# Performance work log

Measured on AMD Instinct MI355X. Metric: run time of the kernel, lower is better.

## Reference

```python
import jax, jax.numpy as jnp
import numpy as np

BN_EPS = 1e-5


def binarize(x):
    # sign binarization with straight-through estimator (identity grad)
    return x + jax.lax.stop_gradient(jnp.sign(x) - x)


def conv2d(x, w, stride):
    # x: [N,C,H,W], w: [O,I,kh,kw], VALID padding (PyTorch default padding=0)
    return jax.lax.conv_general_dilated(
        x, w, window_strides=(stride, stride), padding='VALID',
        dimension_numbers=('NCHW', 'OIHW', 'NCHW'))


def batchnorm(x, gamma, beta, mean, var):
    inv = gamma / jnp.sqrt(var + BN_EPS)          # [C]
    return x * inv[None, :, None, None] + (beta - mean * inv)[None, :, None, None]


def setup_inputs() -> dict:
    key = jax.random.key(0)
    ks = jax.random.split(key, 20)
    B = 8192
    f32 = jnp.float32
    d = {
        'x': jax.random.normal(ks[0], (B, 1, 24, 54), f32),
        'conv1_w': jax.random.normal(ks[1], (32, 1, 3, 3), f32) * 0.3,
        'conv1_b': jax.random.normal(ks[2], (32,), f32) * 0.1,
        'bn1_gamma': 1.0 + 0.1 * jax.random.normal(ks[3], (32,), f32),
        'bn1_beta': 0.1 * jax.random.normal(ks[4], (32,), f32),
        'bn1_mean': 0.1 * jax.random.normal(ks[5], (32,), f32),
        'bn1_var': jax.random.uniform(ks[6], (32,), f32, 0.5, 1.5),
        'conv2_w': jax.random.normal(ks[7], (64, 32, 3, 3), f32) * 0.1,
        'conv2_b': jax.random.normal(ks[8], (64,), f32) * 0.1,
        'bn2_gamma': 1.0 + 0.1 * jax.random.normal(ks[9], (64,), f32),
        'bn2_beta': 0.1 * jax.random.normal(ks[10], (64,), f32),
        'bn2_mean': 0.1 * jax.random.normal(ks[11], (64,), f32),
        'bn2_var': jax.random.uniform(ks[12], (64,), f32, 0.5, 1.5),
        'lin_w': jax.random.normal(ks[13], (500, 3840), f32) * 0.02,
        'lin_b': jax.random.normal(ks[14], (500,), f32) * 0.1,
        'out_w': jax.random.normal(ks[15], (10, 500), f32) * 0.05,
        'out_b': jax.random.normal(ks[16], (10,), f32) * 0.1,
    }
    return d


def reference(x, conv1_w, conv1_b, bn1_gamma, bn1_beta, bn1_mean, bn1_var,
              conv2_w, conv2_b, bn2_gamma, bn2_beta, bn2_mean, bn2_var,
              lin_w, lin_b, out_w, out_b):
    # conv1: input channels (1) != 3 -> input binarized; weight binarized; float bias
    h = conv2d(binarize(x), binarize(conv1_w), 2) + conv1_b[None, :, None, None]
    h = jax.nn.relu(batchnorm(h, bn1_gamma, bn1_beta, bn1_mean, bn1_var))  # [B,32,11,26]
    # conv2: input channels (32) != 3 -> input binarized (values in {0,1} post-ReLU)
    h = conv2d(binarize(h), binarize(conv2_w), 2) + conv2_b[None, :, None, None]
    h = jax.nn.relu(batchnorm(h, bn2_gamma, bn2_beta, bn2_mean, bn2_var))  # [B,64,5,12]
    h = h.reshape(-1, 3840)
    # BinarizeLinear: in_features (3840, 500) != 784 -> input binarized
    h = jax.nn.relu(binarize(h) @ binarize(lin_w).T + lin_b[None, :])      # [B,500]
    y = binarize(h) @ binarize(out_w).T + out_b[None, :]                   # [B,10]
    return y
```

## Files before the change

kernel.cpp:

```cpp
#include <hip/hip_runtime.h>
#include <cstdint>

#define BN_EPS 1e-5f

static constexpr int NB = 8192;
static constexpr int JLIN = 500;

typedef int v4i  __attribute__((ext_vector_type(4)));
typedef int v16i __attribute__((ext_vector_type(16)));


__global__ __launch_bounds__(256) void pack_kernel(
    const float* __restrict__ conv1_w, const float* __restrict__ conv1_b,
    const float* __restrict__ conv2_w, const float* __restrict__ conv2_b,
    const float* __restrict__ lin_w, const float* __restrict__ lin_b,
    const float* __restrict__ out_w,
    const float* __restrict__ bn1_g, const float* __restrict__ bn1_b,
    const float* __restrict__ bn1_m, const float* __restrict__ bn1_v,
    const float* __restrict__ bn2_g, const float* __restrict__ bn2_b,
    const float* __restrict__ bn2_m, const float* __restrict__ bn2_v,
    uint4* __restrict__ wbfrag, uint32_t* __restrict__ cdat,
    uint32_t* __restrict__ lut, uint32_t* __restrict__ wout,
    int* __restrict__ Tlin)
{
    __shared__ float    s_c1w[288];
    __shared__ uint32_t s_wp[32];
    __shared__ float    s_inv1[32], s_sh1[32], s_b1[32];

    int tid = threadIdx.x;
    int b   = blockIdx.x;

    if (b < 512) {
        int e  = b * 256 + tid;
        int L  = e & 63;
        int kq = (e >> 6) & 127;
        int jt = e >> 13;
        int j  = jt * 32 + (L & 31);
        int h  = L >> 5;
        uint32_t dd[4] = {0u, 0u, 0u, 0u};
        if (j < JLIN) {
            int c  = kq >> 1, hi = kq & 1;
            int nb = (hi ? 28 : 32) - 16 * h;
            const float* src = lin_w + (size_t)j * 3840 + c * 60 + hi * 32 + 16 * h;
            #pragma unroll
            for (int i = 0; i < 16; ++i) {
                uint32_t byte = 0;
                if (i < nb) byte = (src[i] > 0.0f) ? 0x01u : 0xFFu;
                dd[i >> 2] |= byte << (8 * (i & 3));
            }
        }
        wbfrag[e] = make_uint4(dd[0], dd[1], dd[2], dd[3]);
        return;
    }

    int mb = b - 512;
    if (mb < 2) {
        for (int i = tid; i < 288; i += 256) s_c1w[i] = conv1_w[i];
        __syncthreads();
        if (tid < 32) {
            uint32_t wp = 0;
            for (int t = 0; t < 9; ++t)
                wp |= (s_c1w[tid * 9 + t] < 0.0f ? 1u : 0u) << t;
            s_wp[tid] = wp;
            float inv = bn1_g[tid] / sqrtf(bn1_v[tid] + BN_EPS);
            s_inv1[tid] = inv;
            s_sh1[tid]  = bn1_b[tid] - bn1_m[tid] * inv;
            s_b1[tid]   = conv1_b[tid];
        }
        __syncthreads();
        uint32_t px = (uint32_t)(mb * 256 + tid);
        uint32_t word = 0;
        for (int c = 0; c < 32; ++c) {
            int d = 9 - 2 * __popc(px ^ s_wp[c]);
            float z = __fadd_rn((float)d, s_b1[c]);
            z = __fadd_rn(__fmul_rn(z, s_inv1[c]), s_sh1[c]);
            word |= (z > 0.0f ? 1u : 0u) << c;
        }
        lut[px] = word;
        return;
    }

    int idx = (mb - 2) * 256 + tid;
    if (idx < 576) {
        int c = idx / 9, tap = idx % 9;
        uint32_t w = 0;
        for (int ic = 0; ic < 32; ++ic)
            w |= (conv2_w[c * 288 + ic * 9 + tap] > 0.0f ? 1u : 0u) << ic;
        float inv = bn2_g[c] / sqrtf(bn2_v[c] + BN_EPS);
        if (inv < 0.0f) w = ~w;
        cdat[tap * 64 + c] = w;
    } else if (idx < 576 + 64) {
        int c = idx - 576;
        float inv = bn2_g[c] / sqrtf(bn2_v[c] + BN_EPS);
        float sh  = bn2_b[c] - bn2_m[c] * inv;
        float b2  = conv2_b[c];
        int T = 10000;
        for (int u = -300; u <= 300; ++u) {
            float v = (inv < 0.0f) ? (float)(-u) : (float)u;
            float z = __fadd_rn(__fmul_rn(__fadd_rn(v, b2), inv), sh);
            if (z > 0.0f) { T = u; break; }
        }
        cdat[576 + c] = (uint32_t)T;
    } else if (idx < 576 + 64 + 512) {
        int j = idx - (576 + 64);
        int T = 10000;
        if (j < JLIN) {
            float lb = lin_b[j];
            int base = (int)floorf(-lb) - 2;
            for (int u = base; u <= base + 5; ++u)
                if (__fadd_rn((float)u, lb) > 0.0f) { T = u; break; }
        }
        Tlin[j] = T;
    } else if (idx < 576 + 64 + 512 + 160) {
        int t = idx - (576 + 64 + 512);
        int j = t >> 4, k = t & 15;
        uint32_t w = 0;
        for (int bb = 0; bb < 32; ++bb) {
            int jj = k * 32 + bb;
            if (jj < JLIN) w |= (out_w[j * 500 + jj] > 0.0f ? 1u : 0u) << bb;
        }
        wout[t] = w;
    }
}

__global__ __launch_bounds__(256) void conv_kernel(
    const float* __restrict__ x,
    const uint32_t* __restrict__ cdat,
    const uint32_t* __restrict__ lut,
    uint32_t* __restrict__ h2b, int* __restrict__ Bs)
{
    __shared__ __align__(8) uint32_t s_flat[4][44];
    __shared__ uint32_t s_lut[512];
    __shared__ __align__(8) uint32_t s_in[4][288];
    __shared__ uint32_t s_base[4][64];

    int tid  = threadIdx.x;
    int lane = tid & 63;
    int wv   = tid >> 6;
    int s    = blockIdx.x * 4 + wv;

    s_lut[tid]       = lut[tid];
    s_lut[tid + 256] = lut[tid + 256];

    const float* xs = x + (size_t)s * 1296;
    #pragma unroll
    for (int it = 0; it < 21; ++it) {
        int f = it * 64 + lane;
        float v = (f < 1296) ? xs[f] : 1.0f;
        uint64_t mk = __ballot(v < 0.0f);
        if (lane == 0) *((uint64_t*)&s_flat[wv][2 * it]) = mk;
    }
    __syncthreads();

    for (int i = tid; i < 4 * 286; i += 256) {
        int sl = i / 286, p = i - sl * 286;
        int oy = p / 26, ox = p - oy * 26;
        uint32_t pxb = 0;
        #pragma unroll
        for (int ky = 0; ky < 3; ++ky) {
            int bitpos = 54 * (2 * oy + ky) + 2 * ox;
            int d  = bitpos >> 5;
            int sh = bitpos & 31;
            uint64_t wp = (uint64_t)s_flat[sl][d] | ((uint64_t)s_flat[sl][d + 1] << 32);
            pxb |= (((uint32_t)(wp >> sh)) & 7u) << (3 * ky);
        }
        s_in[sl][p] = s_lut[pxb];
    }
    __syncthreads();

    for (int i = tid; i < 4 * 60; i += 256) {
        int sl = i / 60, p = i - sl * 60;
        int oy = p / 12, ox = p - 12 * oy;
        uint32_t sum = 0;
        #pragma unroll
        for (int ky = 0; ky < 3; ++ky) {
            const uint32_t* rp = &s_in[sl][(2 * oy + ky) * 26 + 2 * ox];
            sum += __popc(rp[0]) + __popc(rp[1]) + __popc(rp[2]);
        }
        s_base[sl][p] = sum;
    }
    __syncthreads();

    int c = lane;
    uint32_t m[9];
    #pragma unroll
    for (int q = 0; q < 9; ++q) m[q] = cdat[q * 64 + c];
    int T = (int)cdat[576 + c];

    uint64_t acc = 0;
    for (int oy = 0; oy < 5; ++oy) {
        int P[12];
        #pragma unroll
        for (int ox = 0; ox < 12; ++ox) P[ox] = 0;
        #pragma unroll
        for (int ky = 0; ky < 3; ++ky) {
            const uint32_t* rp = &s_in[wv][(2 * oy + ky) * 26];
            uint32_t r[25];
            #pragma unroll
            for (int d = 0; d < 12; ++d)
                *(uint64_t*)&r[2 * d] = *(const uint64_t*)&rp[2 * d];
            r[24] = rp[24];
            uint32_t m0 = m[ky * 3 + 0], m1 = m[ky * 3 + 1], m2 = m[ky * 3 + 2];
            #pragma unroll
            for (int ox = 0; ox < 12; ++ox) {
                P[ox] += __popc(r[2 * ox]     & m0);
                P[ox] += __popc(r[2 * ox + 1] & m1);
                P[ox] += __popc(r[2 * ox + 2] & m2);
            }
        }
        const uint32_t* bp = &s_base[wv][oy * 12];
        uint32_t bits = 0;
        #pragma unroll
        for (int ox = 0; ox < 12; ++ox) {
            int v = 2 * P[ox] - (int)bp[ox];
            bits |= (v >= T ? 1u : 0u) << ox;
        }
        acc |= (uint64_t)bits << (12 * oy);
    }
    uint32_t w0 = (uint32_t)acc;
    uint32_t w1 = (uint32_t)(acc >> 32) & 0x0FFFFFFFu;

    int bsum = __popc(w0) + __popc(w1);
    #pragma unroll
    for (int off = 32; off > 0; off >>= 1) bsum += __shfl_xor(bsum, off, 64);
    if (lane == 0) Bs[s] = bsum;

    *(uint2*)(h2b + (size_t)s * 128 + 2 * c) = make_uint2(w0, w1);
}

__global__ __launch_bounds__(256) void lin2_kernel(
    const uint32_t* __restrict__ h2b,
    const uint4* __restrict__ wbfrag,
    const int* __restrict__ Tlin,
    uint32_t* __restrict__ h3w)
{
    __shared__ uint8_t As[64 * 520];

    int tid  = threadIdx.x;
    int lane = tid & 63;
    int wv   = __builtin_amdgcn_readfirstlane((int)(tid >> 6));
    int sblk = blockIdx.x >> 2;
    int jgrp = blockIdx.x & 3;
    int jt   = jgrp * 4 + wv;
    int s0   = sblk * 64;

    int T = Tlin[jt * 32 + (lane & 31)];
    int row  = lane & 31;
    int half = lane >> 5;

    v16i acc0 = {};
    v16i acc1 = {};

    for (int chunk = 0; chunk < 8; ++chunk) {
        for (int e = tid; e < 1024; e += 256) {
            int sm = e >> 4, wl = e & 15;
            uint32_t w = h2b[(size_t)(s0 + sm) * 128 + chunk * 16 + wl];
            uint32_t dw[8];
            #pragma unroll
            for (int q = 0; q < 8; ++q)
                dw[q] = (((w >> (4 * q)) & 0xFu) * 0x204081u) & 0x01010101u;
            uint64_t* dst = (uint64_t*)(As + sm * 520 + wl * 32);
            dst[0] = (uint64_t)dw[0] | ((uint64_t)dw[1] << 32);
            dst[1] = (uint64_t)dw[2] | ((uint64_t)dw[3] << 32);
            dst[2] = (uint64_t)dw[4] | ((uint64_t)dw[5] << 32);
            dst[3] = (uint64_t)dw[6] | ((uint64_t)dw[7] << 32);
        }
        __syncthreads();

        const uint4* bsrc = wbfrag + ((size_t)jt * 128 + chunk * 16) * 64 + lane;
        #pragma unroll 4
        for (int kq = 0; kq < 16; ++kq) {
            uint4 bw = bsrc[kq * 64];
            v4i bf = {(int)bw.x, (int)bw.y, (int)bw.z, (int)bw.w};
            const uint8_t* ap = As + row * 520 + kq * 32 + half * 16;
            uint64_t lo0 = *(const uint64_t*)ap;
            uint64_t hi0 = *(const uint64_t*)(ap + 8);
            const uint8_t* aq = ap + 32 * 520;
            uint64_t lo1 = *(const uint64_t*)aq;
            uint64_t hi1 = *(const uint64_t*)(aq + 8);
            v4i a0 = {(int)(uint32_t)lo0, (int)(lo0 >> 32),
                      (int)(uint32_t)hi0, (int)(hi0 >> 32)};
            v4i a1 = {(int)(uint32_t)lo1, (int)(lo1 >> 32),
                      (int)(uint32_t)hi1, (int)(hi1 >> 32)};
            acc0 = __builtin_amdgcn_mfma_i32_32x32x32_i8(a0, bf, acc0, 0, 0, 0);
            acc1 = __builtin_amdgcn_mfma_i32_32x32x32_i8(a1, bf, acc1, 0, 0, 0);
        }
        __syncthreads();
    }

    #pragma unroll
    for (int r = 0; r < 16; ++r) {
        int row0 = (r & 3) + 8 * (r >> 2);
        uint64_t mk0 = __ballot(acc0[r] >= T);
        uint64_t mk1 = __ballot(acc1[r] >= T);
        if (lane == 0) {
            h3w[(size_t)(s0 + row0) * 16 + jt]          = (uint32_t)mk0;
            h3w[(size_t)(s0 + row0 + 4) * 16 + jt]      = (uint32_t)(mk0 >> 32);
            h3w[(size_t)(s0 + 32 + row0) * 16 + jt]     = (uint32_t)mk1;
            h3w[(size_t)(s0 + 32 + row0 + 4) * 16 + jt] = (uint32_t)(mk1 >> 32);
        }
    }
}

__global__ __launch_bounds__(256) void out_kernel(
    const uint32_t* __restrict__ h3w,
    const uint32_t* __restrict__ wout,
    const float* __restrict__ out_b,
    float* __restrict__ out)
{
    int s = blockIdx.x * 256 + threadIdx.x;
    const uint4* hp = (const uint4*)(h3w + (size_t)s * 16);
    uint4 q0 = hp[0], q1 = hp[1], q2 = hp[2], q3 = hp[3];
    uint32_t w[16] = {q0.x, q0.y, q0.z, q0.w, q1.x, q1.y, q1.z, q1.w,
                      q2.x, q2.y, q2.z, q2.w, q3.x, q3.y, q3.z, q3.w};
    int B = 0;
    #pragma unroll
    for (int k = 0; k < 16; ++k) B += __popc(w[k]);
    #pragma unroll
    for (int o = 0; o < 10; ++o) {
        int P = 0;
        #pragma unroll
        for (int k = 0; k < 16; ++k) P += __popc(w[k] & wout[o * 16 + k]);
        out[(size_t)s * 10 + o] = __fadd_rn((float)(2 * P - B), out_b[o]);
    }
}

extern "C" void kernel_launch(void* const* d_in, const int* in_sizes, int n_in,
                              void* d_out, int out_size, void* d_ws, size_t ws_size,
                              hipStream_t stream)
{
    const float* x       = (const float*)d_in[0];
    const float* conv1_w = (const float*)d_in[1];
    const float* conv1_b = (const float*)d_in[2];
    const float* bn1_g   = (const float*)d_in[3];
    const float* bn1_b   = (const float*)d_in[4];
    const float* bn1_m   = (const float*)d_in[5];
    const float* bn1_v   = (const float*)d_in[6];
    const float* conv2_w = (const float*)d_in[7];
    const float* conv2_b = (const float*)d_in[8];
    const float* bn2_g   = (const float*)d_in[9];
    const float* bn2_b   = (const float*)d_in[10];
    const float* bn2_m   = (const float*)d_in[11];
    const float* bn2_v   = (const float*)d_in[12];
    const float* lin_w   = (const float*)d_in[13];
    const float* lin_b   = (const float*)d_in[14];
    const float* out_w   = (const float*)d_in[15];
    const float* out_b   = (const float*)d_in[16];

    char* ws = (char*)d_ws;
    uint32_t* h2b    = (uint32_t*)(ws + 0);
    uint4*    wbfrag = (uint4*)   (ws + 4194304);
    uint32_t* h3w    = (uint32_t*)(ws + 6291456);
    uint32_t* cdat   = (uint32_t*)(ws + 6815744);
    uint32_t* lut    = (uint32_t*)(ws + 6818304);
    uint32_t* wout   = (uint32_t*)(ws + 6820352);
    int*      Tlin   = (int*)     (ws + 6820992);
    int*      Bs     = (int*)     (ws + 6823040);

    pack_kernel<<<520, 256, 0, stream>>>(conv1_w, conv1_b, conv2_w, conv2_b,
                                         lin_w, lin_b, out_w,
                                         bn1_g, bn1_b, bn1_m, bn1_v,
                                         bn2_g, bn2_b, bn2_m, bn2_v,
                                         wbfrag, cdat, lut, wout, Tlin);
    conv_kernel<<<NB / 4, 256, 0, stream>>>(x, cdat, lut, h2b, Bs);
    lin2_kernel<<<512, 256, 0, stream>>>(h2b, wbfrag, Tlin, h3w);
    out_kernel<<<32, 256, 0, stream>>>(h3w, wout, out_b, (float*)d_out);
}
```

Measured before the change: 194.8 us.

## Move binary conv2 onto int8 MFMA with prepacked ±1 weight fragments

```diff
diff --git a/kernel.cpp b/kernel.cpp
--- a/kernel.cpp
+++ b/kernel.cpp
@@ -21,7 +21,7 @@
     const float* __restrict__ bn2_m, const float* __restrict__ bn2_v,
     uint4* __restrict__ wbfrag, uint32_t* __restrict__ cdat,
     uint32_t* __restrict__ lut, uint32_t* __restrict__ wout,
-    int* __restrict__ Tlin)
+    int* __restrict__ Tlin, uint4* __restrict__ wcfrag)
 {
     __shared__ float    s_c1w[288];
     __shared__ uint32_t s_wp[32];
@@ -50,6 +50,28 @@
             }
         }
         wbfrag[e] = make_uint4(dd[0], dd[1], dd[2], dd[3]);
+        return;
+    }
+
+    if (b >= 520) {
+        int e = (b - 520) * 256 + tid;
+        if (e < 1152) {
+            int t = e >> 7;
+            int n = (e >> 6) & 1;
+            int L = e & 63;
+            int c = n * 32 + (L & 31);
+            int hb = L >> 5;
+            bool flip = (bn2_g[c] < 0.0f);
+            uint32_t dd[4] = {0u, 0u, 0u, 0u};
+            #pragma unroll
+            for (int i = 0; i < 16; ++i) {
+                int ic = 16 * hb + i;
+                float w = conv2_w[c * 288 + ic * 9 + t];
+                uint32_t byte = ((w > 0.0f) == flip) ? 0xFFu : 0x01u;
+                dd[i >> 2] |= byte << (8 * (i & 3));
+            }
+            wcfrag[e] = make_uint4(dd[0], dd[1], dd[2], dd[3]);
+        }
         return;
     }
 
@@ -127,34 +149,38 @@
     const float* __restrict__ x,
     const uint32_t* __restrict__ cdat,
     const uint32_t* __restrict__ lut,
-    uint32_t* __restrict__ h2b, int* __restrict__ Bs)
-{
-    __shared__ __align__(8) uint32_t s_flat[4][44];
+    const uint4* __restrict__ wcfrag,
+    uint32_t* __restrict__ h2b)
+{
+    __shared__ __align__(16) uint8_t s_bytes[2 * 286 * 32];
     __shared__ uint32_t s_lut[512];
-    __shared__ __align__(8) uint32_t s_in[4][288];
-    __shared__ uint32_t s_base[4][64];
+    __shared__ __align__(8) uint32_t s_flat[2][44];
+    __shared__ uint64_t s_bal[2][2][2][16];
 
     int tid  = threadIdx.x;
     int lane = tid & 63;
     int wv   = tid >> 6;
-    int s    = blockIdx.x * 4 + wv;
+    int s0   = blockIdx.x * 2;
 
     s_lut[tid]       = lut[tid];
     s_lut[tid + 256] = lut[tid + 256];
 
-    const float* xs = x + (size_t)s * 1296;
-    #pragma unroll
-    for (int it = 0; it < 21; ++it) {
-        int f = it * 64 + lane;
-        float v = (f < 1296) ? xs[f] : 1.0f;
-        uint64_t mk = __ballot(v < 0.0f);
-        if (lane == 0) *((uint64_t*)&s_flat[wv][2 * it]) = mk;
+    {
+        int psl = wv >> 1, ph = wv & 1;
+        const float* xs = x + (size_t)(s0 + psl) * 1296;
+        int it0 = ph * 11, it1 = ph ? 21 : 11;
+        for (int it = it0; it < it1; ++it) {
+            int f = it * 64 + lane;
+            float v = (f < 1296) ? xs[f] : 1.0f;
+            uint64_t mk = __ballot(v < 0.0f);
+            if (lane == 0) *((uint64_t*)&s_flat[psl][2 * it]) = mk;
+        }
     }
     __syncthreads();
 
-    for (int i = tid; i < 4 * 286; i += 256) {
-        int sl = i / 286, p = i - sl * 286;
-        int oy = p / 26, ox = p - oy * 26;
+    for (int i = tid; i < 2 * 286; i += 256) {
+        int sl = i / 286, wnd = i - sl * 286;
+        int oy = wnd / 26, ox = wnd - oy * 26;
         uint32_t pxb = 0;
         #pragma unroll
         for (int ky = 0; ky < 3; ++ky) {
@@ -164,68 +190,69 @@
             uint64_t wp = (uint64_t)s_flat[sl][d] | ((uint64_t)s_flat[sl][d + 1] << 32);
             pxb |= (((uint32_t)(wp >> sh)) & 7u) << (3 * ky);
         }
-        s_in[sl][p] = s_lut[pxb];
+        uint32_t w = s_lut[pxb];
+        uint32_t dw[8];
+        #pragma unroll
+        for (int q = 0; q < 8; ++q)
+            dw[q] = (((w >> (4 * q)) & 0xFu) * 0x204081u) & 0x01010101u;
+        uint4* dst = (uint4*)(s_bytes + ((size_t)sl * 286 + wnd) * 32);
+        dst[0] = make_uint4(dw[0], dw[1], dw[2], dw[3]);
+        dst[1] = make_uint4(dw[4], dw[5], dw[6], dw[7]);
     }
     __syncthreads();
 
-    for (int i = tid; i < 4 * 60; i += 256) {
-        int sl = i / 60, p = i - sl * 60;
+    {
+        int sl = wv >> 1, rt = wv & 1;
+        int p = rt * 32 + (lane & 31);
+        if (p > 59) p = 59;
         int oy = p / 12, ox = p - 12 * oy;
-        uint32_t sum = 0;
-        #pragma unroll
-        for (int ky = 0; ky < 3; ++ky) {
-            const uint32_t* rp = &s_in[sl][(2 * oy + ky) * 26 + 2 * ox];
-            sum += __popc(rp[0]) + __popc(rp[1]) + __popc(rp[2]);
-        }
-        s_base[sl][p] = sum;
+        int hb = lane >> 5;
+        const uint8_t* abase = s_bytes + ((size_t)sl * 286 + 52 * oy + 2 * ox) * 32 + 16 * hb;
+        const uint4* bbase = wcfrag + lane;
+
+        v16i acc0 = {};
+        v16i acc1 = {};
+        #pragma unroll
+        for (int t = 0; t < 9; ++t) {
+            const int koff = (t / 3) * 26 + (t % 3);
+            uint4 av = *(const uint4*)(abase + koff * 32);
+            v4i af = {(int)av.x, (int)av.y, (int)av.z, (int)av.w};
+            uint4 b0 = bbase[t * 128];
+            uint4 b1 = bbase[t * 128 + 64];
+            v4i bf0 = {(int)b0.x, (int)b0.y, (int)b0.z, (int)b0.w};
+            v4i bf1 = {(int)b1.x, (int)b1.y, (int)b1.z, (int)b1.w};
+            acc0 = __builtin_amdgcn_mfma_i32_32x32x32_i8(af, bf0, acc0, 0, 0, 0);
+            acc1 = __builtin_amdgcn_mfma_i32_32x32x32_i8(af, bf1, acc1, 0, 0, 0);
+        }
+
+        int T0 = (int)cdat[576 + (lane & 31)];
+        int T1 = (int)cdat[576 + 32 + (lane & 31)];
+        #pragma unroll
+        for (int r = 0; r < 16; ++r) {
+            uint64_t m0 = __ballot(acc0[r] >= T0);
+            uint64_t m1 = __ballot(acc1[r] >= T1);
+            if (lane == 0) {
+                s_bal[sl][rt][0][r] = m0;
+                s_bal[sl][rt][1][r] = m1;
+            }
+        }
     }
     __syncthreads();
 
-    int c = lane;
-    uint32_t m[9];
-    #pragma unroll
-    for (int q = 0; q < 9; ++q) m[q] = cdat[q * 64 + c];
-    int T = (int)cdat[576 + c];
-
-    uint64_t acc = 0;
-    for (int oy = 0; oy < 5; ++oy) {
-        int P[12];
-        #pragma unroll
-        for (int ox = 0; ox < 12; ++ox) P[ox] = 0;
-        #pragma unroll
-        for (int ky = 0; ky < 3; ++ky) {
-            const uint32_t* rp = &s_in[wv][(2 * oy + ky) * 26];
-            uint32_t r[25];
-            #pragma unroll
-            for (int d = 0; d < 12; ++d)
-                *(uint64_t*)&r[2 * d] = *(const uint64_t*)&rp[2 * d];
-            r[24] = rp[24];
-            uint32_t m0 = m[ky * 3 + 0], m1 = m[ky * 3 + 1], m2 = m[ky * 3 + 2];
-            #pragma unroll
-            for (int ox = 0; ox < 12; ++ox) {
-                P[ox] += __popc(r[2 * ox]     & m0);
-                P[ox] += __popc(r[2 * ox + 1] & m1);
-                P[ox] += __popc(r[2 * ox + 2] & m2);
-            }
-        }
-        const uint32_t* bp = &s_base[wv][oy * 12];
-        uint32_t bits = 0;
-        #pragma unroll
-        for (int ox = 0; ox < 12; ++ox) {
-            int v = 2 * P[ox] - (int)bp[ox];
-            bits |= (v >= T ? 1u : 0u) << ox;
-        }
-        acc |= (uint64_t)bits << (12 * oy);
-    }
-    uint32_t w0 = (uint32_t)acc;
-    uint32_t w1 = (uint32_t)(acc >> 32) & 0x0FFFFFFFu;
-
-    int bsum = __popc(w0) + __popc(w1);
-    #pragma unroll
-    for (int off = 32; off > 0; off >>= 1) bsum += __shfl_xor(bsum, off, 64);
-    if (lane == 0) Bs[s] = bsum;
-
-    *(uint2*)(h2b + (size_t)s * 128 + 2 * c) = make_uint2(w0, w1);
+    if (tid < 128) {
+        int esl = tid >> 6, c = tid & 63;
+        int n = c >> 5, cc = c & 31;
+        uint32_t w0 = 0, w1 = 0;
+        #pragma unroll 4
+        for (int p = 0; p < 60; ++p) {
+            int rt = p >> 5, row = p & 31;
+            int hh = (row >> 2) & 1;
+            int r  = (row & 3) | ((row >> 3) << 2);
+            uint32_t bit = (uint32_t)((s_bal[esl][rt][n][r] >> (cc + 32 * hh)) & 1u);
+            if (p < 32) w0 |= bit << p; else w1 |= bit << (p - 32);
+        }
+        *(uint2*)(h2b + (size_t)(s0 + esl) * 128 + 2 * c) = make_uint2(w0, w1);
+    }
 }
 
 __global__ __launch_bounds__(256) void lin2_kernel(
@@ -355,14 +382,14 @@
     uint32_t* lut    = (uint32_t*)(ws + 6818304);
     uint32_t* wout   = (uint32_t*)(ws + 6820352);
     int*      Tlin   = (int*)     (ws + 6820992);
-    int*      Bs     = (int*)     (ws + 6823040);
-
-    pack_kernel<<<520, 256, 0, stream>>>(conv1_w, conv1_b, conv2_w, conv2_b,
+    uint4*    wcfrag = (uint4*)   (ws + 6855808);
+
+    pack_kernel<<<525, 256, 0, stream>>>(conv1_w, conv1_b, conv2_w, conv2_b,
                                          lin_w, lin_b, out_w,
                                          bn1_g, bn1_b, bn1_m, bn1_v,
                                          bn2_g, bn2_b, bn2_m, bn2_v,
-                                         wbfrag, cdat, lut, wout, Tlin);
-    conv_kernel<<<NB / 4, 256, 0, stream>>>(x, cdat, lut, h2b, Bs);
+                                         wbfrag, cdat, lut, wout, Tlin, wcfrag);
+    conv_kernel<<<NB / 2, 256, 0, stream>>>(x, cdat, lut, wcfrag, h2b);
     lin2_kernel<<<512, 256, 0, stream>>>(h2b, wbfrag, Tlin, h3w);
     out_kernel<<<32, 256, 0, stream>>>(h3w, wout, out_b, (float*)d_out);
 }
```

New measurement: 190.5 us. -2.2%, faster.
